# Kernel optimization log

Hardware: AMD Instinct MI355X
Metric: run time of the kernel (lower is better)

The kernel has to match this reference:

```python
import jax, jax.numpy as jnp
import numpy as np
from jax import lax

H = 64  # hidden size of both LSTM layers


def _lstm(x, W_ih, W_hh, b_ih, b_hh):
    """Single-layer batch-first LSTM (torch gate order i,f,g,o).
    x: [B,S,F]; returns (all_h [B,S,H], last_h [B,H])."""
    B, S, _ = x.shape
    # Precompute input projections for all timesteps at once: [B,S,4H]
    xp = jnp.einsum('bsf,gf->bsg', x, W_ih) + b_ih + b_hh

    def step(carry, xt):  # xt: [B,4H]
        h, c = carry
        z = xt + h @ W_hh.T
        i, f, g, o = jnp.split(z, 4, axis=-1)
        i = jax.nn.sigmoid(i)
        f = jax.nn.sigmoid(f)
        g = jnp.tanh(g)
        o = jax.nn.sigmoid(o)
        c = f * c + i * g
        h = o * jnp.tanh(c)
        return (h, c), h

    h0 = jnp.zeros((B, H), x.dtype)
    c0 = jnp.zeros((B, H), x.dtype)
    (h_last, _), hs = lax.scan(step, (h0, c0), jnp.swapaxes(xp, 0, 1))
    return jnp.swapaxes(hs, 0, 1), h_last


def setup_inputs() -> dict:
    key = jax.random.key(0)
    ks = jax.random.split(key, 14)
    B, S, F, OUT = 4096, 512, 1, 24
    s = 1.0 / np.sqrt(H)  # torch default uniform bound ~ 1/sqrt(hidden)
    r = lambda k, shape: jax.random.uniform(k, shape, jnp.float32, -s, s)
    return {
        'x': jax.random.normal(ks[0], (B, S, F), jnp.float32),
        'W_ih1': r(ks[1], (4 * H, F)),
        'W_hh1': r(ks[2], (4 * H, H)),
        'b_ih1': r(ks[3], (4 * H,)),
        'b_hh1': r(ks[4], (4 * H,)),
        'W_ih2': r(ks[5], (4 * H, H)),
        'W_hh2': r(ks[6], (4 * H, H)),
        'b_ih2': r(ks[7], (4 * H,)),
        'b_hh2': r(ks[8], (4 * H,)),
        'W_d1': r(ks[9], (32, H)),
        'b_d1': r(ks[10], (32,)),
        'W_d2': r(ks[11], (OUT, 32)),
        'b_d2': r(ks[12], (OUT,)),
    }


def reference(x, W_ih1, W_hh1, b_ih1, b_hh1, W_ih2, W_hh2, b_ih2, b_hh2,
              W_d1, b_d1, W_d2, b_d2):
    h1, _ = _lstm(x, W_ih1, W_hh1, b_ih1, b_hh1)          # [B,S,64]
    # dropout1 is identity in eval mode
    _, h_last = _lstm(h1, W_ih2, W_hh2, b_ih2, b_hh2)     # [B,64]
    # dropout2 is identity in eval mode
    y = jax.nn.relu(h_last @ W_d1.T + b_d1)                # [B,32]
    return y @ W_d2.T + b_d2                               # [B,24]
```

## Files before the change

kernel.cpp:

```cpp
#include <hip/hip_runtime.h>


typedef __attribute__((ext_vector_type(8))) short bf16x8;
typedef __attribute__((ext_vector_type(4))) float floatx4;

#define SEQ 512
#define HID 64
#define LOG2E 1.4426950408889634f

__device__ inline floatx4 MFMA(bf16x8 a, bf16x8 b, floatx4 c) {
    return __builtin_amdgcn_mfma_f32_16x16x32_bf16(a, b, c, 0, 0, 0);
}
__device__ inline short f2bf(float f) {
    __bf16 b = (__bf16)f;
    return __builtin_bit_cast(short, b);
}
__device__ inline float exp2_fast(float x) {
#if __has_builtin(__builtin_amdgcn_exp2f)
    return __builtin_amdgcn_exp2f(x);
#else
    return __expf(x * 0.6931471805599453f);
#endif
}
__device__ inline float rcp_fast(float x) { return __builtin_amdgcn_rcpf(x); }

__device__ inline float lstm_gate(float zi, float zf, float zg, float zo, float& c) {
    float ei = exp2_fast(zi);
    float ef = exp2_fast(zf);
    float eg = exp2_fast(zg);
    float eo = exp2_fast(zo);
    float P  = (1.0f + ei) * (1.0f + eg);
    float F  = 1.0f + ef;
    float num = c * P + (1.0f - eg) * F;
    c = num * rcp_fast(P * F);
    float ec = exp2_fast(fminf(c * (-2.0f * LOG2E), 40.0f));
    return (1.0f - ec) * rcp_fast((1.0f + eo) * (1.0f + ec));
}

__global__ __launch_bounds__(512, 2) void lstm_fused(
    const float* __restrict__ x,
    const float* __restrict__ Wih1, const float* __restrict__ Whh1,
    const float* __restrict__ bih1, const float* __restrict__ bhh1,
    const float* __restrict__ Wih2, const float* __restrict__ Whh2,
    const float* __restrict__ bih2, const float* __restrict__ bhh2,
    const float* __restrict__ Wd1,  const float* __restrict__ bd1,
    const float* __restrict__ Wd2,  const float* __restrict__ bd2,
    float* __restrict__ out)
{
    const int tid  = threadIdx.x;
    const int wave = tid >> 6;
    const int ct   = wave & 3;
    const int is2  = wave >> 2;
    const int lane = tid & 63;
    const int l15  = lane & 15;
    const int quad = lane >> 4;
    const int b0   = blockIdx.x * 16;

    __shared__ __align__(16) float x_s[16][516];
    __shared__ __align__(16) short h1_s[2][16][72];
    __shared__ __align__(16) short h2_s[2][16][72];
    __shared__ float y1_s[16][32];

    {
        const int row = tid >> 5;
        const int c0  = (tid & 31) * 16;
        const float4* src = reinterpret_cast<const float4*>(x + (size_t)(b0 + row) * SEQ + c0);
        float4* dst = reinterpret_cast<float4*>(&x_s[row][c0]);
        #pragma unroll
        for (int j = 0; j < 4; ++j) dst[j] = src[j];
    }
    for (int i = tid; i < 2 * 16 * 72; i += 512) {
        (&h1_s[0][0][0])[i] = 0;
        (&h2_s[0][0][0])[i] = 0;
    }

    bf16x8 Wf[4][4];
    float wxc[4], bcs[4];
    #pragma unroll
    for (int g = 0; g < 4; ++g) {
        const float sc = (g == 2) ? (-2.0f * LOG2E) : (-LOG2E);
        const int col = g * 64 + ct * 16 + l15;
        if (!is2) {
            wxc[g] = Wih1[col] * sc;
            bcs[g] = (bih1[col] + bhh1[col]) * sc;
        } else {
            wxc[g] = 0.0f;
            bcs[g] = (bih2[col] + bhh2[col]) * sc;
        }
        #pragma unroll
        for (int kt = 0; kt < 2; ++kt) {
            const int koff = kt * 32 + quad * 8;
            union { short s[8]; bf16x8 v; } u0, u1;
            #pragma unroll
            for (int j = 0; j < 8; ++j) {
                if (!is2) {
                    u0.s[j] = f2bf(Whh1[col * HID + koff + j] * sc);
                    u1.s[j] = 0;
                } else {
                    u0.s[j] = f2bf(Wih2[col * HID + koff + j] * sc);
                    u1.s[j] = f2bf(Whh2[col * HID + koff + j] * sc);
                }
            }
            Wf[kt][g] = u0.v;
            Wf[2 + kt][g] = u1.v;
        }
    }

    const int hcol = ct * 16 + l15;
    float cst[4] = {0, 0, 0, 0};

    #pragma unroll 2
    for (int t = 0; t < SEQ; ++t) {
        const int pr1 = (t + 1) & 1;
        const int pr2 = t & 1;
        __syncthreads();
        if (!is2) {
            const bf16x8 A1a = *reinterpret_cast<const bf16x8*>(&h1_s[pr1][l15][quad * 8]);
            const bf16x8 A1b = *reinterpret_cast<const bf16x8*>(&h1_s[pr1][l15][32 + quad * 8]);
            floatx4 z[4];
            #pragma unroll
            for (int g = 0; g < 4; ++g)
                #pragma unroll
                for (int r = 0; r < 4; ++r)
                    z[g][r] = x_s[quad * 4 + r][t] * wxc[g] + bcs[g];
            #pragma unroll
            for (int g = 0; g < 4; ++g) {
                z[g] = MFMA(A1a, Wf[0][g], z[g]);
                z[g] = MFMA(A1b, Wf[1][g], z[g]);
            }
            #pragma unroll
            for (int r = 0; r < 4; ++r) {
                float h1v = lstm_gate(z[0][r], z[1][r], z[2][r], z[3][r], cst[r]);
                h1_s[pr2][quad * 4 + r][hcol] = f2bf(h1v);
            }
        } else {
            const bf16x8 A1a = *reinterpret_cast<const bf16x8*>(&h1_s[pr1][l15][quad * 8]);
            const bf16x8 A1b = *reinterpret_cast<const bf16x8*>(&h1_s[pr1][l15][32 + quad * 8]);
            const bf16x8 A2a = *reinterpret_cast<const bf16x8*>(&h2_s[pr2][l15][quad * 8]);
            const bf16x8 A2b = *reinterpret_cast<const bf16x8*>(&h2_s[pr2][l15][32 + quad * 8]);
            floatx4 z[4];
            #pragma unroll
            for (int g = 0; g < 4; ++g)
                z[g] = floatx4{bcs[g], bcs[g], bcs[g], bcs[g]};
            #pragma unroll
            for (int g = 0; g < 4; ++g) {
                z[g] = MFMA(A1a, Wf[0][g], z[g]);
                z[g] = MFMA(A1b, Wf[1][g], z[g]);
                z[g] = MFMA(A2a, Wf[2][g], z[g]);
                z[g] = MFMA(A2b, Wf[3][g], z[g]);
            }
            const float m2 = (t == 0) ? 0.0f : 1.0f;
            #pragma unroll
            for (int r = 0; r < 4; ++r) {
                float cc = cst[r];
                float h2v = lstm_gate(z[0][r], z[1][r], z[2][r], z[3][r], cc) * m2;
                cst[r] = cc * m2;
                h2_s[pr1][quad * 4 + r][hcol] = f2bf(h2v);
            }
        }
    }

    __syncthreads();
    if (is2) {
        const bf16x8 A1a = *reinterpret_cast<const bf16x8*>(&h1_s[1][l15][quad * 8]);
        const bf16x8 A1b = *reinterpret_cast<const bf16x8*>(&h1_s[1][l15][32 + quad * 8]);
        const bf16x8 A2a = *reinterpret_cast<const bf16x8*>(&h2_s[0][l15][quad * 8]);
        const bf16x8 A2b = *reinterpret_cast<const bf16x8*>(&h2_s[0][l15][32 + quad * 8]);
        floatx4 z[4];
        #pragma unroll
        for (int g = 0; g < 4; ++g) {
            z[g] = floatx4{bcs[g], bcs[g], bcs[g], bcs[g]};
            z[g] = MFMA(A1a, Wf[0][g], z[g]);
            z[g] = MFMA(A1b, Wf[1][g], z[g]);
            z[g] = MFMA(A2a, Wf[2][g], z[g]);
            z[g] = MFMA(A2b, Wf[3][g], z[g]);
        }
        float* h2f = &x_s[0][0];
        #pragma unroll
        for (int r = 0; r < 4; ++r) {
            float cc = cst[r];
            float h2v = lstm_gate(z[0][r], z[1][r], z[2][r], z[3][r], cc);
            h2f[(quad * 4 + r) * HID + hcol] = h2v;
        }
    }
    __syncthreads();

    const float* h2f = &x_s[0][0];
    for (int idx = tid; idx < 16 * 32; idx += 512) {
        const int b = idx >> 5, o = idx & 31;
        float acc = bd1[o];
        #pragma unroll 8
        for (int k = 0; k < HID; ++k) acc += h2f[b * HID + k] * Wd1[o * HID + k];
        y1_s[b][o] = fmaxf(acc, 0.0f);
    }
    __syncthreads();
    for (int idx = tid; idx < 16 * 24; idx += 512) {
        const int b = idx / 24, o = idx - b * 24;
        float acc = bd2[o];
        #pragma unroll 8
        for (int k = 0; k < 32; ++k) acc += y1_s[b][k] * Wd2[o * 32 + k];
        out[(size_t)(b0 + b) * 24 + o] = acc;
    }
}

extern "C" void kernel_launch(void* const* d_in, const int* in_sizes, int n_in,
                              void* d_out, int out_size, void* d_ws, size_t ws_size,
                              hipStream_t stream) {
    const float* x    = (const float*)d_in[0];
    const float* Wih1 = (const float*)d_in[1];
    const float* Whh1 = (const float*)d_in[2];
    const float* bih1 = (const float*)d_in[3];
    const float* bhh1 = (const float*)d_in[4];
    const float* Wih2 = (const float*)d_in[5];
    const float* Whh2 = (const float*)d_in[6];
    const float* bih2 = (const float*)d_in[7];
    const float* bhh2 = (const float*)d_in[8];
    const float* Wd1  = (const float*)d_in[9];
    const float* bd1  = (const float*)d_in[10];
    const float* Wd2  = (const float*)d_in[11];
    const float* bd2  = (const float*)d_in[12];
    float* out = (float*)d_out;

    lstm_fused<<<256, 512, 0, stream>>>(x, Wih1, Whh1, bih1, bhh1,
                                        Wih2, Whh2, bih2, bhh2,
                                        Wd1, bd1, Wd2, bd2, out);
}
```

Measured before the change: 465.5 us.

## Replace per-step block barriers with LDS counter flags and 4-deep hidden-state rings

Removes the __syncthreads at every timestep and replaces it with point-to-point waits on per-timestep LDS counters. Layer-1 waves signal when their h1 slice is written, and layer-2 waves signal their h2 slice. A 'done' counter guards reuse of the 4-slot ring buffers that replace the old double buffers. The aim is to let layer-1 and layer-2 waves drift apart instead of lockstepping on a full barrier. The cost is atomic traffic, spin-polling with s_sleep wakeup latency, and a guard-break escape that could silently yield wrong results if a wait times out.

```diff
diff --git a/kernel.cpp b/kernel.cpp
--- a/kernel.cpp
+++ b/kernel.cpp
@@ -35,6 +35,18 @@
     c = num * rcp_fast(P * F);
     float ec = exp2_fast(fminf(c * (-2.0f * LOG2E), 40.0f));
     return (1.0f - ec) * rcp_fast((1.0f + eo) * (1.0f + ec));
+}
+
+__device__ inline void wg_wait(int* addr, int target) {
+    int guard = 0;
+    while (__hip_atomic_load(addr, __ATOMIC_ACQUIRE, __HIP_MEMORY_SCOPE_WORKGROUP) < target) {
+        __builtin_amdgcn_s_sleep(1);
+        if (++guard > (1 << 22)) break;
+    }
+}
+__device__ inline void wg_signal(int* addr) {
+    if ((threadIdx.x & 63) == 0)
+        (void)__hip_atomic_fetch_add(addr, 1, __ATOMIC_RELEASE, __HIP_MEMORY_SCOPE_WORKGROUP);
 }
 
 __global__ __launch_bounds__(512, 2) void lstm_fused(
@@ -57,9 +69,10 @@
     const int b0   = blockIdx.x * 16;
 
     __shared__ __align__(16) float x_s[16][516];
-    __shared__ __align__(16) short h1_s[2][16][72];
-    __shared__ __align__(16) short h2_s[2][16][72];
+    __shared__ __align__(16) short h1_s[4][16][72];
+    __shared__ __align__(16) short h2_s[4][16][72];
     __shared__ float y1_s[16][32];
+    __shared__ int cnt1[SEQ], cnt2[SEQ], done[SEQ];
 
     {
         const int row = tid >> 5;
@@ -69,9 +82,11 @@
         #pragma unroll
         for (int j = 0; j < 4; ++j) dst[j] = src[j];
     }
-    for (int i = tid; i < 2 * 16 * 72; i += 512) {
-        (&h1_s[0][0][0])[i] = 0;
-        (&h2_s[0][0][0])[i] = 0;
+    {
+        int* p1 = (int*)&h1_s[0][0][0];
+        int* p2 = (int*)&h2_s[0][0][0];
+        for (int i = tid; i < 4 * 16 * 72 / 2; i += 512) { p1[i] = 0; p2[i] = 0; }
+        for (int i = tid; i < SEQ; i += 512) { cnt1[i] = 0; cnt2[i] = 0; done[i] = 0; }
     }
 
     bf16x8 Wf[4][4];
@@ -109,14 +124,14 @@
     const int hcol = ct * 16 + l15;
     float cst[4] = {0, 0, 0, 0};
 
-    #pragma unroll 2
+    __syncthreads();
+
     for (int t = 0; t < SEQ; ++t) {
-        const int pr1 = (t + 1) & 1;
-        const int pr2 = t & 1;
-        __syncthreads();
+        const int sr1 = (t + 3) & 3;
         if (!is2) {
-            const bf16x8 A1a = *reinterpret_cast<const bf16x8*>(&h1_s[pr1][l15][quad * 8]);
-            const bf16x8 A1b = *reinterpret_cast<const bf16x8*>(&h1_s[pr1][l15][32 + quad * 8]);
+            if (t > 0) wg_wait(&cnt1[t - 1], 4);
+            const bf16x8 A1a = *reinterpret_cast<const bf16x8*>(&h1_s[sr1][l15][quad * 8]);
+            const bf16x8 A1b = *reinterpret_cast<const bf16x8*>(&h1_s[sr1][l15][32 + quad * 8]);
             floatx4 z[4];
             #pragma unroll
             for (int g = 0; g < 4; ++g)
@@ -128,16 +143,23 @@
                 z[g] = MFMA(A1a, Wf[0][g], z[g]);
                 z[g] = MFMA(A1b, Wf[1][g], z[g]);
             }
-            #pragma unroll
-            for (int r = 0; r < 4; ++r) {
-                float h1v = lstm_gate(z[0][r], z[1][r], z[2][r], z[3][r], cst[r]);
-                h1_s[pr2][quad * 4 + r][hcol] = f2bf(h1v);
-            }
+            float hv[4];
+            #pragma unroll
+            for (int r = 0; r < 4; ++r)
+                hv[r] = lstm_gate(z[0][r], z[1][r], z[2][r], z[3][r], cst[r]);
+            if (t >= 3) wg_wait(&done[t - 3], 8);
+            #pragma unroll
+            for (int r = 0; r < 4; ++r)
+                h1_s[t & 3][quad * 4 + r][hcol] = f2bf(hv[r]);
+            wg_signal(&cnt1[t]);
         } else {
-            const bf16x8 A1a = *reinterpret_cast<const bf16x8*>(&h1_s[pr1][l15][quad * 8]);
-            const bf16x8 A1b = *reinterpret_cast<const bf16x8*>(&h1_s[pr1][l15][32 + quad * 8]);
-            const bf16x8 A2a = *reinterpret_cast<const bf16x8*>(&h2_s[pr2][l15][quad * 8]);
-            const bf16x8 A2b = *reinterpret_cast<const bf16x8*>(&h2_s[pr2][l15][32 + quad * 8]);
+            if (t > 0) wg_wait(&cnt1[t - 1], 4);
+            if (t > 1) wg_wait(&cnt2[t - 2], 4);
+            const int sr2 = (t + 2) & 3;
+            const bf16x8 A1a = *reinterpret_cast<const bf16x8*>(&h1_s[sr1][l15][quad * 8]);
+            const bf16x8 A1b = *reinterpret_cast<const bf16x8*>(&h1_s[sr1][l15][32 + quad * 8]);
+            const bf16x8 A2a = *reinterpret_cast<const bf16x8*>(&h2_s[sr2][l15][quad * 8]);
+            const bf16x8 A2b = *reinterpret_cast<const bf16x8*>(&h2_s[sr2][l15][32 + quad * 8]);
             floatx4 z[4];
             #pragma unroll
             for (int g = 0; g < 4; ++g)
@@ -150,22 +172,31 @@
                 z[g] = MFMA(A2b, Wf[3][g], z[g]);
             }
             const float m2 = (t == 0) ? 0.0f : 1.0f;
+            float hv[4];
             #pragma unroll
             for (int r = 0; r < 4; ++r) {
                 float cc = cst[r];
-                float h2v = lstm_gate(z[0][r], z[1][r], z[2][r], z[3][r], cc) * m2;
+                hv[r] = lstm_gate(z[0][r], z[1][r], z[2][r], z[3][r], cc) * m2;
                 cst[r] = cc * m2;
-                h2_s[pr1][quad * 4 + r][hcol] = f2bf(h2v);
-            }
-        }
-    }
-
-    __syncthreads();
+            }
+            if (t >= 3) wg_wait(&done[t - 3], 8);
+            if (t > 0) {
+                #pragma unroll
+                for (int r = 0; r < 4; ++r)
+                    h2_s[(t + 3) & 3][quad * 4 + r][hcol] = f2bf(hv[r]);
+                wg_signal(&cnt2[t - 1]);
+            }
+        }
+        wg_signal(&done[t]);
+    }
+
     if (is2) {
-        const bf16x8 A1a = *reinterpret_cast<const bf16x8*>(&h1_s[1][l15][quad * 8]);
-        const bf16x8 A1b = *reinterpret_cast<const bf16x8*>(&h1_s[1][l15][32 + quad * 8]);
-        const bf16x8 A2a = *reinterpret_cast<const bf16x8*>(&h2_s[0][l15][quad * 8]);
-        const bf16x8 A2b = *reinterpret_cast<const bf16x8*>(&h2_s[0][l15][32 + quad * 8]);
+        wg_wait(&cnt1[SEQ - 1], 4);
+        wg_wait(&cnt2[SEQ - 2], 4);
+        const bf16x8 A1a = *reinterpret_cast<const bf16x8*>(&h1_s[(SEQ - 1) & 3][l15][quad * 8]);
+        const bf16x8 A1b = *reinterpret_cast<const bf16x8*>(&h1_s[(SEQ - 1) & 3][l15][32 + quad * 8]);
+        const bf16x8 A2a = *reinterpret_cast<const bf16x8*>(&h2_s[(SEQ - 2) & 3][l15][quad * 8]);
+        const bf16x8 A2b = *reinterpret_cast<const bf16x8*>(&h2_s[(SEQ - 2) & 3][l15][32 + quad * 8]);
         floatx4 z[4];
         #pragma unroll
         for (int g = 0; g < 4; ++g) {
@@ -179,8 +210,7 @@
         #pragma unroll
         for (int r = 0; r < 4; ++r) {
             float cc = cst[r];
-            float h2v = lstm_gate(z[0][r], z[1][r], z[2][r], z[3][r], cc);
-            h2f[(quad * 4 + r) * HID + hcol] = h2v;
+            h2f[(quad * 4 + r) * HID + hcol] = lstm_gate(z[0][r], z[1][r], z[2][r], z[3][r], cc);
         }
     }
     __syncthreads();
```

After: 535.9 us. 15.1% more time.

## Split each timestep into two phases overlapping MFMA of one layer with gates of other

Applied to the files above, without the earlier changes.

Restructures the per-timestep loop into two barrier-separated phases. Layer-1 waves do their MFMAs while layer-2 waves evaluate gate nonlinearities, then the roles swap, so matrix and transcendental work from the two layers run at the same time. The layer-2 pipeline is shifted by one step and gains an extra epilogue step. In exchange each timestep now needs two __syncthreads instead of one, and the loop is no longer unrolled.

```diff
diff --git a/kernel.cpp b/kernel.cpp
--- a/kernel.cpp
+++ b/kernel.cpp
@@ -108,64 +108,75 @@
 
     const int hcol = ct * 16 + l15;
     float cst[4] = {0, 0, 0, 0};
-
-    #pragma unroll 2
+    floatx4 zh[4];
+    #pragma unroll
+    for (int g = 0; g < 4; ++g) zh[g] = floatx4{bcs[g], bcs[g], bcs[g], bcs[g]};
+
+    __syncthreads();
+
     for (int t = 0; t < SEQ; ++t) {
-        const int pr1 = (t + 1) & 1;
-        const int pr2 = t & 1;
-        __syncthreads();
+        floatx4 z1[4];
         if (!is2) {
-            const bf16x8 A1a = *reinterpret_cast<const bf16x8*>(&h1_s[pr1][l15][quad * 8]);
-            const bf16x8 A1b = *reinterpret_cast<const bf16x8*>(&h1_s[pr1][l15][32 + quad * 8]);
-            floatx4 z[4];
+            const bf16x8 A1a = *reinterpret_cast<const bf16x8*>(&h1_s[(t + 1) & 1][l15][quad * 8]);
+            const bf16x8 A1b = *reinterpret_cast<const bf16x8*>(&h1_s[(t + 1) & 1][l15][32 + quad * 8]);
             #pragma unroll
             for (int g = 0; g < 4; ++g)
                 #pragma unroll
                 for (int r = 0; r < 4; ++r)
-                    z[g][r] = x_s[quad * 4 + r][t] * wxc[g] + bcs[g];
+                    z1[g][r] = x_s[quad * 4 + r][t] * wxc[g] + bcs[g];
             #pragma unroll
             for (int g = 0; g < 4; ++g) {
-                z[g] = MFMA(A1a, Wf[0][g], z[g]);
-                z[g] = MFMA(A1b, Wf[1][g], z[g]);
-            }
-            #pragma unroll
-            for (int r = 0; r < 4; ++r) {
-                float h1v = lstm_gate(z[0][r], z[1][r], z[2][r], z[3][r], cst[r]);
-                h1_s[pr2][quad * 4 + r][hcol] = f2bf(h1v);
-            }
-        } else {
-            const bf16x8 A1a = *reinterpret_cast<const bf16x8*>(&h1_s[pr1][l15][quad * 8]);
-            const bf16x8 A1b = *reinterpret_cast<const bf16x8*>(&h1_s[pr1][l15][32 + quad * 8]);
-            const bf16x8 A2a = *reinterpret_cast<const bf16x8*>(&h2_s[pr2][l15][quad * 8]);
-            const bf16x8 A2b = *reinterpret_cast<const bf16x8*>(&h2_s[pr2][l15][32 + quad * 8]);
-            floatx4 z[4];
-            #pragma unroll
-            for (int g = 0; g < 4; ++g)
-                z[g] = floatx4{bcs[g], bcs[g], bcs[g], bcs[g]};
-            #pragma unroll
-            for (int g = 0; g < 4; ++g) {
-                z[g] = MFMA(A1a, Wf[0][g], z[g]);
-                z[g] = MFMA(A1b, Wf[1][g], z[g]);
-                z[g] = MFMA(A2a, Wf[2][g], z[g]);
-                z[g] = MFMA(A2b, Wf[3][g], z[g]);
-            }
-            const float m2 = (t == 0) ? 0.0f : 1.0f;
+                z1[g] = MFMA(A1a, Wf[0][g], z1[g]);
+                z1[g] = MFMA(A1b, Wf[1][g], z1[g]);
+            }
+        } else if (t >= 1) {
+            const float m2 = (t >= 2) ? 1.0f : 0.0f;
             #pragma unroll
             for (int r = 0; r < 4; ++r) {
                 float cc = cst[r];
-                float h2v = lstm_gate(z[0][r], z[1][r], z[2][r], z[3][r], cc) * m2;
+                float hv = lstm_gate(zh[0][r], zh[1][r], zh[2][r], zh[3][r], cc) * m2;
                 cst[r] = cc * m2;
-                h2_s[pr1][quad * 4 + r][hcol] = f2bf(h2v);
-            }
-        }
-    }
-
-    __syncthreads();
+                h2_s[t & 1][quad * 4 + r][hcol] = f2bf(hv);
+            }
+        }
+        __syncthreads();
+        if (!is2) {
+            #pragma unroll
+            for (int r = 0; r < 4; ++r) {
+                float hv = lstm_gate(z1[0][r], z1[1][r], z1[2][r], z1[3][r], cst[r]);
+                h1_s[t & 1][quad * 4 + r][hcol] = f2bf(hv);
+            }
+        } else {
+            const bf16x8 A1a = *reinterpret_cast<const bf16x8*>(&h1_s[(t + 1) & 1][l15][quad * 8]);
+            const bf16x8 A1b = *reinterpret_cast<const bf16x8*>(&h1_s[(t + 1) & 1][l15][32 + quad * 8]);
+            const bf16x8 A2a = *reinterpret_cast<const bf16x8*>(&h2_s[t & 1][l15][quad * 8]);
+            const bf16x8 A2b = *reinterpret_cast<const bf16x8*>(&h2_s[t & 1][l15][32 + quad * 8]);
+            #pragma unroll
+            for (int g = 0; g < 4; ++g) {
+                floatx4 z = floatx4{bcs[g], bcs[g], bcs[g], bcs[g]};
+                z = MFMA(A1a, Wf[0][g], z);
+                z = MFMA(A1b, Wf[1][g], z);
+                z = MFMA(A2a, Wf[2][g], z);
+                z = MFMA(A2b, Wf[3][g], z);
+                zh[g] = z;
+            }
+        }
+        __syncthreads();
+    }
+
     if (is2) {
-        const bf16x8 A1a = *reinterpret_cast<const bf16x8*>(&h1_s[1][l15][quad * 8]);
-        const bf16x8 A1b = *reinterpret_cast<const bf16x8*>(&h1_s[1][l15][32 + quad * 8]);
-        const bf16x8 A2a = *reinterpret_cast<const bf16x8*>(&h2_s[0][l15][quad * 8]);
-        const bf16x8 A2b = *reinterpret_cast<const bf16x8*>(&h2_s[0][l15][32 + quad * 8]);
+        #pragma unroll
+        for (int r = 0; r < 4; ++r) {
+            float hv = lstm_gate(zh[0][r], zh[1][r], zh[2][r], zh[3][r], cst[r]);
+            h2_s[SEQ & 1][quad * 4 + r][hcol] = f2bf(hv);
+        }
+    }
+    __syncthreads();
+    if (is2) {
+        const bf16x8 A1a = *reinterpret_cast<const bf16x8*>(&h1_s[(SEQ + 1) & 1][l15][quad * 8]);
+        const bf16x8 A1b = *reinterpret_cast<const bf16x8*>(&h1_s[(SEQ + 1) & 1][l15][32 + quad * 8]);
+        const bf16x8 A2a = *reinterpret_cast<const bf16x8*>(&h2_s[SEQ & 1][l15][quad * 8]);
+        const bf16x8 A2b = *reinterpret_cast<const bf16x8*>(&h2_s[SEQ & 1][l15][32 + quad * 8]);
         floatx4 z[4];
         #pragma unroll
         for (int g = 0; g < 4; ++g) {
@@ -179,8 +190,7 @@
         #pragma unroll
         for (int r = 0; r < 4; ++r) {
             float cc = cst[r];
-            float h2v = lstm_gate(z[0][r], z[1][r], z[2][r], z[3][r], cc);
-            h2f[(quad * 4 + r) * HID + hcol] = h2v;
+            h2f[(quad * 4 + r) * HID + hcol] = lstm_gate(z[0][r], z[1][r], z[2][r], z[3][r], cc);
         }
     }
     __syncthreads();
```

Result: slower. 476.1 us (+2.3%).

## Process 32 batch rows per block with 16 waves and 1024 threads

Applied to the files above, without the earlier changes.

Doubles the batch rows per workgroup to 32 by adding a row-group index, so each block runs 16 waves (8 per LSTM layer) and the grid halves to 128 blocks. This amortizes the per-block weight loading and puts more independent waves on each SIMD to hide MFMA and transcendental latency within the serial time loop. In exchange, only half as many workgroups exist, which may leave compute units idle, and each per-step barrier now spans 16 waves. An extra barrier is also added before the time loop so the shared-memory initialization is complete before it is read.

```diff
diff --git a/kernel.cpp b/kernel.cpp
--- a/kernel.cpp
+++ b/kernel.cpp
@@ -6,6 +6,7 @@
 
 #define SEQ 512
 #define HID 64
+#define ROWS 32
 #define LOG2E 1.4426950408889634f
 
 __device__ inline floatx4 MFMA(bf16x8 a, bf16x8 b, floatx4 c) {
@@ -37,7 +38,7 @@
     return (1.0f - ec) * rcp_fast((1.0f + eo) * (1.0f + ec));
 }
 
-__global__ __launch_bounds__(512, 2) void lstm_fused(
+__global__ __launch_bounds__(1024, 1) void lstm_fused(
     const float* __restrict__ x,
     const float* __restrict__ Wih1, const float* __restrict__ Whh1,
     const float* __restrict__ bih1, const float* __restrict__ bhh1,
@@ -50,16 +51,17 @@
     const int tid  = threadIdx.x;
     const int wave = tid >> 6;
     const int ct   = wave & 3;
-    const int is2  = wave >> 2;
+    const int rg   = (wave >> 2) & 1;
+    const int is2  = wave >> 3;
     const int lane = tid & 63;
     const int l15  = lane & 15;
     const int quad = lane >> 4;
-    const int b0   = blockIdx.x * 16;
-
-    __shared__ __align__(16) float x_s[16][516];
-    __shared__ __align__(16) short h1_s[2][16][72];
-    __shared__ __align__(16) short h2_s[2][16][72];
-    __shared__ float y1_s[16][32];
+    const int b0   = blockIdx.x * ROWS;
+
+    __shared__ __align__(16) float x_s[ROWS][516];
+    __shared__ __align__(16) short h1_s[2][ROWS][72];
+    __shared__ __align__(16) short h2_s[2][ROWS][72];
+    __shared__ float y1_s[ROWS][32];
 
     {
         const int row = tid >> 5;
@@ -69,7 +71,7 @@
         #pragma unroll
         for (int j = 0; j < 4; ++j) dst[j] = src[j];
     }
-    for (int i = tid; i < 2 * 16 * 72; i += 512) {
+    for (int i = tid; i < 2 * ROWS * 72; i += 1024) {
         (&h1_s[0][0][0])[i] = 0;
         (&h2_s[0][0][0])[i] = 0;
     }
@@ -107,7 +109,11 @@
     }
 
     const int hcol = ct * 16 + l15;
+    const int arow = rg * 16 + l15;
+    const int wrow = rg * 16 + quad * 4;
     float cst[4] = {0, 0, 0, 0};
+
+    __syncthreads();
 
     #pragma unroll 2
     for (int t = 0; t < SEQ; ++t) {
@@ -115,14 +121,14 @@
         const int pr2 = t & 1;
         __syncthreads();
         if (!is2) {
-            const bf16x8 A1a = *reinterpret_cast<const bf16x8*>(&h1_s[pr1][l15][quad * 8]);
-            const bf16x8 A1b = *reinterpret_cast<const bf16x8*>(&h1_s[pr1][l15][32 + quad * 8]);
+            const bf16x8 A1a = *reinterpret_cast<const bf16x8*>(&h1_s[pr1][arow][quad * 8]);
+            const bf16x8 A1b = *reinterpret_cast<const bf16x8*>(&h1_s[pr1][arow][32 + quad * 8]);
             floatx4 z[4];
             #pragma unroll
             for (int g = 0; g < 4; ++g)
                 #pragma unroll
                 for (int r = 0; r < 4; ++r)
-                    z[g][r] = x_s[quad * 4 + r][t] * wxc[g] + bcs[g];
+                    z[g][r] = x_s[wrow + r][t] * wxc[g] + bcs[g];
             #pragma unroll
             for (int g = 0; g < 4; ++g) {
                 z[g] = MFMA(A1a, Wf[0][g], z[g]);
@@ -130,14 +136,14 @@
             }
             #pragma unroll
             for (int r = 0; r < 4; ++r) {
-                float h1v = lstm_gate(z[0][r], z[1][r], z[2][r], z[3][r], cst[r]);
-                h1_s[pr2][quad * 4 + r][hcol] = f2bf(h1v);
+                float hv = lstm_gate(z[0][r], z[1][r], z[2][r], z[3][r], cst[r]);
+                h1_s[pr2][wrow + r][hcol] = f2bf(hv);
             }
         } else {
-            const bf16x8 A1a = *reinterpret_cast<const bf16x8*>(&h1_s[pr1][l15][quad * 8]);
-            const bf16x8 A1b = *reinterpret_cast<const bf16x8*>(&h1_s[pr1][l15][32 + quad * 8]);
-            const bf16x8 A2a = *reinterpret_cast<const bf16x8*>(&h2_s[pr2][l15][quad * 8]);
-            const bf16x8 A2b = *reinterpret_cast<const bf16x8*>(&h2_s[pr2][l15][32 + quad * 8]);
+            const bf16x8 A1a = *reinterpret_cast<const bf16x8*>(&h1_s[pr1][arow][quad * 8]);
+            const bf16x8 A1b = *reinterpret_cast<const bf16x8*>(&h1_s[pr1][arow][32 + quad * 8]);
+            const bf16x8 A2a = *reinterpret_cast<const bf16x8*>(&h2_s[pr2][arow][quad * 8]);
+            const bf16x8 A2b = *reinterpret_cast<const bf16x8*>(&h2_s[pr2][arow][32 + quad * 8]);
             floatx4 z[4];
             #pragma unroll
             for (int g = 0; g < 4; ++g)
@@ -153,19 +159,19 @@
             #pragma unroll
             for (int r = 0; r < 4; ++r) {
                 float cc = cst[r];
-                float h2v = lstm_gate(z[0][r], z[1][r], z[2][r], z[3][r], cc) * m2;
+                float hv = lstm_gate(z[0][r], z[1][r], z[2][r], z[3][r], cc) * m2;
                 cst[r] = cc * m2;
-                h2_s[pr1][quad * 4 + r][hcol] = f2bf(h2v);
+                h2_s[pr1][wrow + r][hcol] = f2bf(hv);
             }
         }
     }
 
     __syncthreads();
     if (is2) {
-        const bf16x8 A1a = *reinterpret_cast<const bf16x8*>(&h1_s[1][l15][quad * 8]);
-        const bf16x8 A1b = *reinterpret_cast<const bf16x8*>(&h1_s[1][l15][32 + quad * 8]);
-        const bf16x8 A2a = *reinterpret_cast<const bf16x8*>(&h2_s[0][l15][quad * 8]);
-        const bf16x8 A2b = *reinterpret_cast<const bf16x8*>(&h2_s[0][l15][32 + quad * 8]);
+        const bf16x8 A1a = *reinterpret_cast<const bf16x8*>(&h1_s[1][arow][quad * 8]);
+        const bf16x8 A1b = *reinterpret_cast<const bf16x8*>(&h1_s[1][arow][32 + quad * 8]);
+        const bf16x8 A2a = *reinterpret_cast<const bf16x8*>(&h2_s[0][arow][quad * 8]);
+        const bf16x8 A2b = *reinterpret_cast<const bf16x8*>(&h2_s[0][arow][32 + quad * 8]);
         floatx4 z[4];
         #pragma unroll
         for (int g = 0; g < 4; ++g) {
@@ -179,14 +185,13 @@
         #pragma unroll
         for (int r = 0; r < 4; ++r) {
             float cc = cst[r];
-            float h2v = lstm_gate(z[0][r], z[1][r], z[2][r], z[3][r], cc);
-            h2f[(quad * 4 + r) * HID + hcol] = h2v;
+            h2f[(wrow + r) * HID + hcol] = lstm_gate(z[0][r], z[1][r], z[2][r], z[3][r], cc);
         }
     }
     __syncthreads();
 
     const float* h2f = &x_s[0][0];
-    for (int idx = tid; idx < 16 * 32; idx += 512) {
+    for (int idx = tid; idx < ROWS * 32; idx += 1024) {
         const int b = idx >> 5, o = idx & 31;
         float acc = bd1[o];
         #pragma unroll 8
@@ -194,7 +199,7 @@
         y1_s[b][o] = fmaxf(acc, 0.0f);
     }
     __syncthreads();
-    for (int idx = tid; idx < 16 * 24; idx += 512) {
+    for (int idx = tid; idx < ROWS * 24; idx += 1024) {
         const int b = idx / 24, o = idx - b * 24;
         float acc = bd2[o];
         #pragma unroll 8
@@ -221,7 +226,7 @@
     const float* bd2  = (const float*)d_in[12];
     float* out = (float*)d_out;
 
-    lstm_fused<<<256, 512, 0, stream>>>(x, Wih1, Whh1, bih1, bhh1,
-                                        Wih2, Whh2, bih2, bhh2,
-                                        Wd1, bd1, Wd2, bd2, out);
-}
+    lstm_fused<<<128, 1024, 0, stream>>>(x, Wih1, Whh1, bih1, bhh1,
+                                         Wih2, Whh2, bih2, bhh2,
+                                         Wd1, bd1, Wd2, bd2, out);
+}
```

Result: slower. 1.440 ms (+209.3%).
